# Performance work log

Measured on AMD Instinct MI355X. Metric: run time of the kernel, lower is better.

The kernel has to match this reference:

```python
import jax, jax.numpy as jnp
import numpy as np

VOCAB, EMB, HID, LABELS, SEQ = 30522, 768, 1024, 2, 4096


def setup_inputs() -> dict:
    key = jax.random.key(0)
    ks = jax.random.split(key, 8)
    s = 0.02  # keep gate pre-activations in a sane range
    return {
        "sentence": jax.random.randint(ks[0], (SEQ,), 0, VOCAB),
        "emb": jax.random.normal(ks[1], (VOCAB, EMB), jnp.float32),
        "w_ih": jax.random.normal(ks[2], (4 * HID, EMB), jnp.float32) * s,
        "w_hh": jax.random.normal(ks[3], (4 * HID, HID), jnp.float32) * s,
        "b_ih": jax.random.normal(ks[4], (4 * HID,), jnp.float32) * s,
        "b_hh": jax.random.normal(ks[5], (4 * HID,), jnp.float32) * s,
        "w_out": jax.random.normal(ks[6], (LABELS, HID), jnp.float32) * s,
        "b_out": jax.random.normal(ks[7], (LABELS,), jnp.float32) * s,
    }


def reference(sentence, emb, w_ih, w_hh, b_ih, b_hh, w_out, b_out):
    H = w_hh.shape[1]
    x = emb[sentence]                       # [T, E] frozen embedding lookup
    xg = x @ w_ih.T + (b_ih + b_hh)         # [T, 4H] precompute input-to-gate GEMM

    def cell(carry, xgt):
        h, c = carry
        gates = xgt + w_hh @ h              # [4H]
        i, f, g, o = jnp.split(gates, 4)
        i = jax.nn.sigmoid(i)
        f = jax.nn.sigmoid(f)
        g = jnp.tanh(g)
        o = jax.nn.sigmoid(o)
        c = f * c + i * g
        h = o * jnp.tanh(c)
        return (h, c), None

    h0 = jnp.zeros((H,), x.dtype)
    c0 = jnp.zeros((H,), x.dtype)
    (h_T, _), _ = jax.lax.scan(cell, (h0, c0), xg)
    y = h_T @ w_out.T + b_out               # [label_size]
    return jax.nn.log_softmax(y[None, :], axis=-1)  # [1, label_size]
```

## Files before the change

### kernel.cpp

```cpp
#include <hip/hip_runtime.h>
#include <hip/hip_bf16.h>

#define VOCAB 30522
#define EMB   768
#define HID   1024
#define SEQ   4096
#define NG    4096
#define NWG   128
#define RT    256

static __device__ __forceinline__ unsigned short f32_to_bf16(float f) {
  unsigned u = __float_as_uint(f);
  u = (u + 0x7fffu + ((u >> 16) & 1u)) >> 16;
  return (unsigned short)u;
}

#define BM 64
#define BN 64
#define BK 16

__global__ __launch_bounds__(256) void xg_gemm(
    const int* __restrict__ sent, const float* __restrict__ emb,
    const float* __restrict__ w_ih, const float* __restrict__ b_ih,
    const float* __restrict__ b_hh, unsigned long long* __restrict__ xg64,
    int* __restrict__ flags) {
  __shared__ float As[BK][BM + 4];
  __shared__ float Bs[BK][BN + 4];
  const int tid = threadIdx.x;
  const int n0 = blockIdx.x * BN;
  const int m0 = blockIdx.y * BM;
  const int tx = tid & 15, ty = tid >> 4;
  const int lr = tid >> 2;
  const int lk = (tid & 3) * 4;

  const int arow = sent[m0 + lr];
  const float* aptr = emb + (size_t)arow * EMB + lk;
  const float* bptr = w_ih + (size_t)(n0 + lr) * EMB + lk;

  float acc[4][4] = {};

  for (int k0 = 0; k0 < EMB; k0 += BK) {
    float4 av = *(const float4*)(aptr + k0);
    float4 bv = *(const float4*)(bptr + k0);
    __syncthreads();
    As[lk + 0][lr] = av.x; As[lk + 1][lr] = av.y;
    As[lk + 2][lr] = av.z; As[lk + 3][lr] = av.w;
    Bs[lk + 0][lr] = bv.x; Bs[lk + 1][lr] = bv.y;
    Bs[lk + 2][lr] = bv.z; Bs[lk + 3][lr] = bv.w;
    __syncthreads();
#pragma unroll
    for (int k = 0; k < BK; ++k) {
      float4 a = *(const float4*)&As[k][ty * 4];
      float4 b = *(const float4*)&Bs[k][tx * 4];
      acc[0][0] = fmaf(a.x, b.x, acc[0][0]); acc[0][1] = fmaf(a.x, b.y, acc[0][1]);
      acc[0][2] = fmaf(a.x, b.z, acc[0][2]); acc[0][3] = fmaf(a.x, b.w, acc[0][3]);
      acc[1][0] = fmaf(a.y, b.x, acc[1][0]); acc[1][1] = fmaf(a.y, b.y, acc[1][1]);
      acc[1][2] = fmaf(a.y, b.z, acc[1][2]); acc[1][3] = fmaf(a.y, b.w, acc[1][3]);
      acc[2][0] = fmaf(a.z, b.x, acc[2][0]); acc[2][1] = fmaf(a.z, b.y, acc[2][1]);
      acc[2][2] = fmaf(a.z, b.z, acc[2][2]); acc[2][3] = fmaf(a.z, b.w, acc[2][3]);
      acc[3][0] = fmaf(a.w, b.x, acc[3][0]); acc[3][1] = fmaf(a.w, b.y, acc[3][1]);
      acc[3][2] = fmaf(a.w, b.z, acc[3][2]); acc[3][3] = fmaf(a.w, b.w, acc[3][3]);
    }
  }

  const int gbase = n0 + tx * 4;
  const float b0 = b_ih[gbase]     + b_hh[gbase];
  const float b1 = b_ih[gbase + 1] + b_hh[gbase + 1];
  const float b2 = b_ih[gbase + 2] + b_hh[gbase + 2];
  const float b3 = b_ih[gbase + 3] + b_hh[gbase + 3];
#pragma unroll
  for (int i = 0; i < 4; ++i) {
    const int gm = m0 + ty * 4 + i;
    unsigned lo = ((unsigned)f32_to_bf16(acc[i][1] + b1) << 16) |
                  (unsigned)f32_to_bf16(acc[i][0] + b0);
    unsigned hi = ((unsigned)f32_to_bf16(acc[i][3] + b3) << 16) |
                  (unsigned)f32_to_bf16(acc[i][2] + b2);
    unsigned long long wrd = ((unsigned long long)hi << 32) | lo;
    __hip_atomic_store(xg64 + (size_t)gm * (NG / 4) + (gbase >> 2), wrd,
                       __ATOMIC_RELAXED, __HIP_MEMORY_SCOPE_AGENT);
  }
  __syncthreads();
  if (tid == 0)
    __hip_atomic_fetch_add(flags + blockIdx.y, 1,
                           __ATOMIC_RELAXED, __HIP_MEMORY_SCOPE_AGENT);
}

__global__ __launch_bounds__(RT, 1) void lstm_rec(
    const float* __restrict__ w_hh, const unsigned* __restrict__ xg32,
    unsigned long long* __restrict__ slots, int* __restrict__ flags) {
  __shared__ unsigned hl[2][512];

  const int tid  = threadIdx.x;
  const int wg   = blockIdx.x;
  const int lane = tid & 63;
  const int wv   = tid >> 6;
  const int c    = lane;
  const int m    = lane & 1;

  unsigned wp[8][8];
#pragma unroll
  for (int s = 0; s < 8; ++s) {
    const int q = s >> 1, mm = s & 1;
    const int gr = q * HID + wg * 8 + 2 * wv + mm;
    const float* wr = w_hh + (size_t)gr * HID;
#pragma unroll
    for (int k = 0; k < 8; ++k) {
      float2 wv2 = *(const float2*)(wr + 2 * (c + 64 * k));
      wp[s][k] = ((unsigned)f32_to_bf16(wv2.y) << 16) | (unsigned)f32_to_bf16(wv2.x);
    }
  }
#pragma unroll
  for (int s = 0; s < 8; ++s)
#pragma unroll
    for (int k = 0; k < 8; ++k)
      asm volatile("" : "+v"(wp[s][k]));

  if (lane == 0)
    __hip_atomic_store(slots + (wg * 4 + wv), 0ULL,
                       __ATOMIC_RELAXED, __HIP_MEMORY_SCOPE_AGENT);
  if (wv == 0) {
    while (__hip_atomic_load(flags, __ATOMIC_RELAXED, __HIP_MEMORY_SCOPE_AGENT) < 64) {}
  }
  __syncthreads();

  float cst = 0.f;

  for (int t = 0; t < SEQ; ++t) {
    float xqv = 0.f;
    if (lane < 8) {
      const int q = lane >> 1;
      unsigned w = __hip_atomic_load(
          xg32 + ((size_t)t * (NG / 2) + q * (HID / 2) + wg * 4 + wv),
          __ATOMIC_RELAXED, __HIP_MEMORY_SCOPE_AGENT);
      xqv = __uint_as_float((lane & 1) ? (w & 0xffff0000u) : (w << 16));
    }

    if (wv == 0) {
      if (((t + 1) & 63) == 0 && (t + 1) < SEQ) {
        const int nb = (t + 1) >> 6;
        while (__hip_atomic_load(flags + nb, __ATOMIC_RELAXED,
                                 __HIP_MEMORY_SCOPE_AGENT) < 64) {}
      }
      const unsigned long long want = (unsigned long long)t;
      unsigned long long* sb = slots + ((t & 1) << 9);
      unsigned long long v[8];
      for (;;) {
#pragma unroll
        for (int k = 0; k < 8; ++k)
          v[k] = __hip_atomic_load(sb + 64 * k + lane,
                                   __ATOMIC_RELAXED, __HIP_MEMORY_SCOPE_AGENT);
        bool ok = true;
#pragma unroll
        for (int k = 0; k < 8; ++k) ok &= ((v[k] >> 32) == want);
        if (ok) break;
      }
#pragma unroll
      for (int k = 0; k < 8; ++k)
        hl[t & 1][64 * k + lane] = (unsigned)v[k];
    }
    __syncthreads();

    const unsigned* hb = hl[t & 1];
    float hx[8], hy[8];
#pragma unroll
    for (int k = 0; k < 8; ++k) {
      unsigned hw = hb[c + 64 * k];
      hx[k] = __uint_as_float(hw << 16);
      hy[k] = __uint_as_float(hw & 0xffff0000u);
    }

    float acc[8];
#pragma unroll
    for (int s = 0; s < 8; ++s) {
      float a = 0.f;
#pragma unroll
      for (int k = 0; k < 8; ++k) {
        unsigned w = wp[s][k];
        a = fmaf(__uint_as_float(w << 16),         hx[k], a);
        a = fmaf(__uint_as_float(w & 0xffff0000u), hy[k], a);
      }
      acc[s] = a;
    }

#pragma unroll
    for (int M = 1, n = 8; M <= 4; M <<= 1, n >>= 1) {
#pragma unroll
      for (int j = 0; j < 4; ++j) {
        if (j < (n >> 1)) {
          float u  = (lane & M) ? acc[2 * j + 1] : acc[2 * j];
          float u2 = (lane & M) ? acc[2 * j]     : acc[2 * j + 1];
          acc[j] = u + __shfl_xor(u2, M, 64);
        }
      }
    }
    float r = acc[0];
    r += __shfl_xor(r, 8, 64);
    r += __shfl_xor(r, 16, 64);
    r += __shfl_xor(r, 32, 64);

    {
      const int s = lane & 7;
      const bool isg = (s >> 1) == 2;
      float z = r + xqv;
      z = isg ? 2.f * z : z;
      float sg = 1.f / (1.f + __expf(-z));
      r = isg ? fmaf(2.f, sg, -1.f) : sg;
    }

    float i_ = __shfl(r, m,     64);
    float f_ = __shfl(r, 2 + m, 64);
    float g_ = __shfl(r, 4 + m, 64);
    float o_ = __shfl(r, 6 + m, 64);

    cst = fmaf(f_, cst, i_ * g_);
    float th = fmaf(2.f, 1.f / (1.f + __expf(-2.f * cst)), -1.f);
    float hn = o_ * th;

    float hn1 = __shfl(hn, 1, 64);
    if (lane == 0) {
      unsigned payload = ((unsigned)f32_to_bf16(hn1) << 16) | (unsigned)f32_to_bf16(hn);
      unsigned long long pv =
          ((unsigned long long)(unsigned)(t + 1) << 32) | (unsigned long long)payload;
      __hip_atomic_store(slots + (((t + 1) & 1) << 9) + (wg * 4 + wv), pv,
                         __ATOMIC_RELAXED, __HIP_MEMORY_SCOPE_AGENT);
    }
  }
}

__global__ __launch_bounds__(256) void head_kernel(
    const unsigned long long* __restrict__ hslots, const float* __restrict__ w_out,
    const float* __restrict__ b_out, float* __restrict__ out) {
  __shared__ float s0[256], s1[256];
  const int tid = threadIdx.x;
  float p0 = 0.f, p1 = 0.f;
  for (int w = tid; w < 512; w += 256) {
    unsigned pw = (unsigned)hslots[w];
    float h0 = __uint_as_float(pw << 16);
    float h1 = __uint_as_float(pw & 0xffff0000u);
    p0 = fmaf(h0, w_out[2 * w], fmaf(h1, w_out[2 * w + 1], p0));
    p1 = fmaf(h0, w_out[HID + 2 * w], fmaf(h1, w_out[HID + 2 * w + 1], p1));
  }
  s0[tid] = p0; s1[tid] = p1;
  __syncthreads();
  for (int off = 128; off; off >>= 1) {
    if (tid < off) { s0[tid] += s0[tid + off]; s1[tid] += s1[tid + off]; }
    __syncthreads();
  }
  if (tid == 0) {
    float y0 = s0[0] + b_out[0], y1 = s1[0] + b_out[1];
    float mx = fmaxf(y0, y1);
    float lse = mx + logf(expf(y0 - mx) + expf(y1 - mx));
    out[0] = y0 - lse;
    out[1] = y1 - lse;
  }
}

extern "C" void kernel_launch(void* const* d_in, const int* in_sizes, int n_in,
                              void* d_out, int out_size, void* d_ws, size_t ws_size,
                              hipStream_t stream) {
  const int*   sent  = (const int*)d_in[0];
  const float* emb   = (const float*)d_in[1];
  const float* w_ih  = (const float*)d_in[2];
  const float* w_hh  = (const float*)d_in[3];
  const float* b_ih  = (const float*)d_in[4];
  const float* b_hh  = (const float*)d_in[5];
  const float* w_out = (const float*)d_in[6];
  const float* b_out = (const float*)d_in[7];
  float* out = (float*)d_out;

  unsigned long long* slots = (unsigned long long*)d_ws;
  int* flags = (int*)((char*)d_ws + 8192);
  void* xg   = (char*)d_ws + 16384;

  hipMemsetAsync(flags, 0, 256, stream);

  dim3 ggrid(NG / BN, SEQ / BM);
  xg_gemm<<<ggrid, 256, 0, stream>>>(sent, emb, w_ih, b_ih, b_hh,
                                     (unsigned long long*)xg, flags);

  lstm_rec<<<NWG, RT, 0, stream>>>(w_hh, (const unsigned*)xg, slots, flags);

  head_kernel<<<1, 256, 0, stream>>>(slots, w_out, b_out, out);
}
```

Before: 7.499 ms.

## Fuse input GEMM and LSTM recurrence into one persistent kernel with worker blocks

Merges the xg GEMM and recurrent kernels into a single launch: the first 128 blocks run the recurrence while 128 extra blocks loop over GEMM tiles and signal per-row-block flags. The recurrence can then start as soon as the first time-step rows are ready, overlapping the GEMM with the serial scan instead of depending on the previous kernel's launch order and residency. The risk is that the GEMM gets fewer blocks (128 persistent workers instead of the full grid), so if the recurrence outpaces tile production it stalls on flags. Residency of all 256 blocks is assumed, which the spin-waiting needs to avoid deadlock.

```diff
diff --git a/kernel.cpp b/kernel.cpp
--- a/kernel.cpp
+++ b/kernel.cpp
@@ -7,6 +7,7 @@
 #define SEQ   4096
 #define NG    4096
 #define NWG   128
+#define NWORK 128
 #define RT    256
 
 static __device__ __forceinline__ unsigned short f32_to_bf16(float f) {
@@ -19,79 +20,85 @@
 #define BN 64
 #define BK 16
 
-__global__ __launch_bounds__(256) void xg_gemm(
+__global__ __launch_bounds__(RT, 1) void fused_lstm(
     const int* __restrict__ sent, const float* __restrict__ emb,
     const float* __restrict__ w_ih, const float* __restrict__ b_ih,
-    const float* __restrict__ b_hh, unsigned long long* __restrict__ xg64,
+    const float* __restrict__ b_hh, const float* __restrict__ w_hh,
+    unsigned long long* __restrict__ xg64, unsigned long long* __restrict__ slots,
     int* __restrict__ flags) {
-  __shared__ float As[BK][BM + 4];
-  __shared__ float Bs[BK][BN + 4];
+  __shared__ union {
+    struct { float As[BK][BM + 4]; float Bs[BK][BN + 4]; } g;
+    unsigned hl[2][512];
+  } sm;
+
+  const int blk = blockIdx.x;
   const int tid = threadIdx.x;
-  const int n0 = blockIdx.x * BN;
-  const int m0 = blockIdx.y * BM;
-  const int tx = tid & 15, ty = tid >> 4;
-  const int lr = tid >> 2;
-  const int lk = (tid & 3) * 4;
-
-  const int arow = sent[m0 + lr];
-  const float* aptr = emb + (size_t)arow * EMB + lk;
-  const float* bptr = w_ih + (size_t)(n0 + lr) * EMB + lk;
-
-  float acc[4][4] = {};
-
-  for (int k0 = 0; k0 < EMB; k0 += BK) {
-    float4 av = *(const float4*)(aptr + k0);
-    float4 bv = *(const float4*)(bptr + k0);
-    __syncthreads();
-    As[lk + 0][lr] = av.x; As[lk + 1][lr] = av.y;
-    As[lk + 2][lr] = av.z; As[lk + 3][lr] = av.w;
-    Bs[lk + 0][lr] = bv.x; Bs[lk + 1][lr] = bv.y;
-    Bs[lk + 2][lr] = bv.z; Bs[lk + 3][lr] = bv.w;
-    __syncthreads();
-#pragma unroll
-    for (int k = 0; k < BK; ++k) {
-      float4 a = *(const float4*)&As[k][ty * 4];
-      float4 b = *(const float4*)&Bs[k][tx * 4];
-      acc[0][0] = fmaf(a.x, b.x, acc[0][0]); acc[0][1] = fmaf(a.x, b.y, acc[0][1]);
-      acc[0][2] = fmaf(a.x, b.z, acc[0][2]); acc[0][3] = fmaf(a.x, b.w, acc[0][3]);
-      acc[1][0] = fmaf(a.y, b.x, acc[1][0]); acc[1][1] = fmaf(a.y, b.y, acc[1][1]);
-      acc[1][2] = fmaf(a.y, b.z, acc[1][2]); acc[1][3] = fmaf(a.y, b.w, acc[1][3]);
-      acc[2][0] = fmaf(a.z, b.x, acc[2][0]); acc[2][1] = fmaf(a.z, b.y, acc[2][1]);
-      acc[2][2] = fmaf(a.z, b.z, acc[2][2]); acc[2][3] = fmaf(a.z, b.w, acc[2][3]);
-      acc[3][0] = fmaf(a.w, b.x, acc[3][0]); acc[3][1] = fmaf(a.w, b.y, acc[3][1]);
-      acc[3][2] = fmaf(a.w, b.z, acc[3][2]); acc[3][3] = fmaf(a.w, b.w, acc[3][3]);
-    }
-  }
-
-  const int gbase = n0 + tx * 4;
-  const float b0 = b_ih[gbase]     + b_hh[gbase];
-  const float b1 = b_ih[gbase + 1] + b_hh[gbase + 1];
-  const float b2 = b_ih[gbase + 2] + b_hh[gbase + 2];
-  const float b3 = b_ih[gbase + 3] + b_hh[gbase + 3];
-#pragma unroll
-  for (int i = 0; i < 4; ++i) {
-    const int gm = m0 + ty * 4 + i;
-    unsigned lo = ((unsigned)f32_to_bf16(acc[i][1] + b1) << 16) |
-                  (unsigned)f32_to_bf16(acc[i][0] + b0);
-    unsigned hi = ((unsigned)f32_to_bf16(acc[i][3] + b3) << 16) |
-                  (unsigned)f32_to_bf16(acc[i][2] + b2);
-    unsigned long long wrd = ((unsigned long long)hi << 32) | lo;
-    __hip_atomic_store(xg64 + (size_t)gm * (NG / 4) + (gbase >> 2), wrd,
-                       __ATOMIC_RELAXED, __HIP_MEMORY_SCOPE_AGENT);
-  }
-  __syncthreads();
-  if (tid == 0)
-    __hip_atomic_fetch_add(flags + blockIdx.y, 1,
+
+  if (blk >= NWG) {
+    const int widx = blk - NWG;
+    const int tx = tid & 15, ty = tid >> 4;
+    const int lr = tid >> 2;
+    const int lk = (tid & 3) * 4;
+
+    for (int tile = widx; tile < (SEQ / BM) * (NG / BN); tile += NWORK) {
+      const int m0 = (tile >> 6) * BM;
+      const int n0 = (tile & 63) * BN;
+
+      const int arow = sent[m0 + lr];
+      const float* aptr = emb + (size_t)arow * EMB + lk;
+      const float* bptr = w_ih + (size_t)(n0 + lr) * EMB + lk;
+
+      float acc[4][4] = {};
+      for (int k0 = 0; k0 < EMB; k0 += BK) {
+        float4 av = *(const float4*)(aptr + k0);
+        float4 bv = *(const float4*)(bptr + k0);
+        __syncthreads();
+        sm.g.As[lk + 0][lr] = av.x; sm.g.As[lk + 1][lr] = av.y;
+        sm.g.As[lk + 2][lr] = av.z; sm.g.As[lk + 3][lr] = av.w;
+        sm.g.Bs[lk + 0][lr] = bv.x; sm.g.Bs[lk + 1][lr] = bv.y;
+        sm.g.Bs[lk + 2][lr] = bv.z; sm.g.Bs[lk + 3][lr] = bv.w;
+        __syncthreads();
+#pragma unroll
+        for (int k = 0; k < BK; ++k) {
+          float4 a = *(const float4*)&sm.g.As[k][ty * 4];
+          float4 b = *(const float4*)&sm.g.Bs[k][tx * 4];
+          acc[0][0] = fmaf(a.x, b.x, acc[0][0]); acc[0][1] = fmaf(a.x, b.y, acc[0][1]);
+          acc[0][2] = fmaf(a.x, b.z, acc[0][2]); acc[0][3] = fmaf(a.x, b.w, acc[0][3]);
+          acc[1][0] = fmaf(a.y, b.x, acc[1][0]); acc[1][1] = fmaf(a.y, b.y, acc[1][1]);
+          acc[1][2] = fmaf(a.y, b.z, acc[1][2]); acc[1][3] = fmaf(a.y, b.w, acc[1][3]);
+          acc[2][0] = fmaf(a.z, b.x, acc[2][0]); acc[2][1] = fmaf(a.z, b.y, acc[2][1]);
+          acc[2][2] = fmaf(a.z, b.z, acc[2][2]); acc[2][3] = fmaf(a.z, b.w, acc[2][3]);
+          acc[3][0] = fmaf(a.w, b.x, acc[3][0]); acc[3][1] = fmaf(a.w, b.y, acc[3][1]);
+          acc[3][2] = fmaf(a.w, b.z, acc[3][2]); acc[3][3] = fmaf(a.w, b.w, acc[3][3]);
+        }
+      }
+
+      const int gbase = n0 + tx * 4;
+      const float b0 = b_ih[gbase]     + b_hh[gbase];
+      const float b1 = b_ih[gbase + 1] + b_hh[gbase + 1];
+      const float b2 = b_ih[gbase + 2] + b_hh[gbase + 2];
+      const float b3 = b_ih[gbase + 3] + b_hh[gbase + 3];
+#pragma unroll
+      for (int i = 0; i < 4; ++i) {
+        const int gm = m0 + ty * 4 + i;
+        unsigned lo = ((unsigned)f32_to_bf16(acc[i][1] + b1) << 16) |
+                      (unsigned)f32_to_bf16(acc[i][0] + b0);
+        unsigned hi = ((unsigned)f32_to_bf16(acc[i][3] + b3) << 16) |
+                      (unsigned)f32_to_bf16(acc[i][2] + b2);
+        unsigned long long wrd = ((unsigned long long)hi << 32) | lo;
+        __hip_atomic_store(xg64 + (size_t)gm * (NG / 4) + (gbase >> 2), wrd,
                            __ATOMIC_RELAXED, __HIP_MEMORY_SCOPE_AGENT);
-}
-
-__global__ __launch_bounds__(RT, 1) void lstm_rec(
-    const float* __restrict__ w_hh, const unsigned* __restrict__ xg32,
-    unsigned long long* __restrict__ slots, int* __restrict__ flags) {
-  __shared__ unsigned hl[2][512];
-
-  const int tid  = threadIdx.x;
-  const int wg   = blockIdx.x;
+      }
+      __syncthreads();
+      if (tid == 0)
+        __hip_atomic_fetch_add(flags + (tile >> 6), 1,
+                               __ATOMIC_RELAXED, __HIP_MEMORY_SCOPE_AGENT);
+    }
+    return;
+  }
+
+  const unsigned* xg32 = (const unsigned*)xg64;
+  const int wg   = blk;
   const int lane = tid & 63;
   const int wv   = tid >> 6;
   const int c    = lane;
@@ -156,11 +163,11 @@
       }
 #pragma unroll
       for (int k = 0; k < 8; ++k)
-        hl[t & 1][64 * k + lane] = (unsigned)v[k];
+        sm.hl[t & 1][64 * k + lane] = (unsigned)v[k];
     }
     __syncthreads();
 
-    const unsigned* hb = hl[t & 1];
+    const unsigned* hb = sm.hl[t & 1];
     float hx[8], hy[8];
 #pragma unroll
     for (int k = 0; k < 8; ++k) {
@@ -274,11 +281,9 @@
 
   hipMemsetAsync(flags, 0, 256, stream);
 
-  dim3 ggrid(NG / BN, SEQ / BM);
-  xg_gemm<<<ggrid, 256, 0, stream>>>(sent, emb, w_ih, b_ih, b_hh,
-                                     (unsigned long long*)xg, flags);
-
-  lstm_rec<<<NWG, RT, 0, stream>>>(w_hh, (const unsigned*)xg, slots, flags);
+  fused_lstm<<<NWG + NWORK, RT, 0, stream>>>(
+      sent, emb, w_ih, b_ih, b_hh, w_hh,
+      (unsigned long long*)xg, slots, flags);
 
   head_kernel<<<1, 256, 0, stream>>>(slots, w_out, b_out, out);
 }
```

Measured after the change: 7.215 ms. 3.8% less time.
